# Kernel tuning notes

Measured on AMD Instinct MI355X. Metric: run time of the kernel, lower is better.

The kernel has to match this reference:

```python
import jax, jax.numpy as jnp
import numpy as np

L, E, NH, V, BS = 8, 1024, 16, 32000, 1024  # layers, embed, heads, vocab, block_size
HD = E // NH  # head dim = 64
FF = 4 * E


def layernorm(x, scale, bias, eps=1e-5):
    mu = jnp.mean(x, axis=-1, keepdims=True)
    var = jnp.var(x, axis=-1, keepdims=True)
    return (x - mu) * jax.lax.rsqrt(var + eps) * scale + bias


def setup_inputs() -> dict:
    key = jax.random.key(0)
    ks = jax.random.split(key, 16)
    s = 0.02
    B, T = 2, 1024
    return {
        "idx": jax.random.randint(ks[0], (B, T), 0, V),
        "tok_emb": jax.random.normal(ks[1], (V, E), jnp.float32) * s,
        "pos_emb": jax.random.normal(ks[2], (BS, E), jnp.float32) * s,
        "Wq": jax.random.normal(ks[3], (L, E, E), jnp.float32) * s,
        "Wk": jax.random.normal(ks[4], (L, E, E), jnp.float32) * s,
        "Wv": jax.random.normal(ks[5], (L, E, E), jnp.float32) * s,
        "Wo": jax.random.normal(ks[6], (L, E, E), jnp.float32) * s,
        "bo": jnp.zeros((L, E), jnp.float32),
        "ln1_s": jnp.ones((L, E), jnp.float32),
        "ln1_b": jnp.zeros((L, E), jnp.float32),
        "W1": jax.random.normal(ks[7], (L, E, FF), jnp.float32) * s,
        "b1": jnp.zeros((L, FF), jnp.float32),
        "W2": jax.random.normal(ks[8], (L, FF, E), jnp.float32) * s,
        "b2": jnp.zeros((L, E), jnp.float32),
        "ln2_s": jnp.ones((L, E), jnp.float32),
        "ln2_b": jnp.zeros((L, E), jnp.float32),
        "lnf_s": jnp.ones((E,), jnp.float32),
        "lnf_b": jnp.zeros((E,), jnp.float32),
        "lm_w": jax.random.normal(ks[9], (E, V), jnp.float32) * s,
        "lm_b": jnp.zeros((V,), jnp.float32),
    }


def reference(idx, tok_emb, pos_emb, Wq, Wk, Wv, Wo, bo, ln1_s, ln1_b,
              W1, b1, W2, b2, ln2_s, ln2_b, lnf_s, lnf_b, lm_w, lm_b):
    B, T = idx.shape
    x = tok_emb[idx] + pos_emb[:T]  # [B,T,E]
    causal = jnp.triu(jnp.ones((T, T), bool), 1)  # True above diagonal -> masked
    scale = 1.0 / jnp.sqrt(jnp.asarray(HD, x.dtype))
    for l in range(L):
        h = layernorm(x, ln1_s[l], ln1_b[l])
        q = (h @ Wq[l]).reshape(B, T, NH, HD)
        k = (h @ Wk[l]).reshape(B, T, NH, HD)
        v = (h @ Wv[l]).reshape(B, T, NH, HD)
        scores = jnp.einsum("bthd,bshd->bhts", q, k) * scale  # [B,H,T,T]
        scores = jnp.where(causal, -jnp.inf, scores)
        attn = jax.nn.softmax(scores, axis=-1)
        o = jnp.einsum("bhts,bshd->bthd", attn, v).reshape(B, T, E)
        x = x + o @ Wo[l] + bo[l]
        h2 = layernorm(x, ln2_s[l], ln2_b[l])
        x = x + jax.nn.gelu(h2 @ W1[l] + b1[l], approximate=False) @ W2[l] + b2[l]
    x = layernorm(x, lnf_s, lnf_b)
    logits = x @ lm_w + lm_b  # [B,T,V]
    return logits
```

## Files before the change

### kernel.cpp

```cpp
#include <hip/hip_runtime.h>

#define EDIM 1024
#define NHEADS 16
#define HDIM 64
#define TSEQ 1024
#define NBATCH 2
#define MROWS 2048
#define FFDIM 4096
#define NLAYERS 8
#define VOCAB 32000
#define QKVN 3072

typedef __attribute__((ext_vector_type(4))) float f32x4;
typedef __attribute__((ext_vector_type(8))) short short8;

__device__ __forceinline__ unsigned short f2bf(float f) {
    union { float f; unsigned u; } v; v.f = f;
    unsigned r = v.u + 0x7fffu + ((v.u >> 16) & 1u);
    return (unsigned short)(r >> 16);
}

__device__ __forceinline__ f32x4 mfma_bf16(short8 a, short8 b, f32x4 c) {
    return __builtin_amdgcn_mfma_f32_16x16x32_bf16(a, b, c, 0, 0, 0);
}

__device__ __forceinline__ void gload16(const unsigned short* g, unsigned short* l) {
    __builtin_amdgcn_global_load_lds(
        (const __attribute__((address_space(1))) unsigned int*)g,
        (__attribute__((address_space(3))) unsigned int*)l, 16, 0, 0);
}

__global__ __launch_bounds__(256) void embed_kernel(
    const int* __restrict__ idx, const float* __restrict__ tok,
    const float* __restrict__ pos, float* __restrict__ x)
{
    int row = blockIdx.x;
    int t = row & (TSEQ - 1);
    int tokid = idx[row];
    const float* tp = tok + (size_t)tokid * EDIM;
    const float* pp = pos + (size_t)t * EDIM;
    float* xp = x + (size_t)row * EDIM;
    int c = threadIdx.x * 4;
    f32x4 a = *(const f32x4*)(tp + c);
    f32x4 b = *(const f32x4*)(pp + c);
    *(f32x4*)(xp + c) = a + b;
}

__device__ __forceinline__ void ln_store(
    f32x4 v, int tid, const float* __restrict__ sc, const float* __restrict__ bi,
    unsigned short* __restrict__ hrow)
{
    float sum = v[0] + v[1] + v[2] + v[3];
    float sq = v[0]*v[0] + v[1]*v[1] + v[2]*v[2] + v[3]*v[3];
    #pragma unroll
    for (int m = 1; m <= 32; m <<= 1) { sum += __shfl_xor(sum, m); sq += __shfl_xor(sq, m); }
    __shared__ float sh[8];
    int w = tid >> 6;
    if ((tid & 63) == 0) { sh[w] = sum; sh[4 + w] = sq; }
    __syncthreads();
    sum = sh[0] + sh[1] + sh[2] + sh[3];
    sq  = sh[4] + sh[5] + sh[6] + sh[7];
    float mu = sum * (1.0f / EDIM);
    float inv = rsqrtf(sq * (1.0f / EDIM) - mu * mu + 1e-5f);
    int c = tid * 4;
    unsigned o0 = (unsigned)f2bf((v[0] - mu) * inv * sc[c + 0] + bi[c + 0])
                | ((unsigned)f2bf((v[1] - mu) * inv * sc[c + 1] + bi[c + 1]) << 16);
    unsigned o1 = (unsigned)f2bf((v[2] - mu) * inv * sc[c + 2] + bi[c + 2])
                | ((unsigned)f2bf((v[3] - mu) * inv * sc[c + 3] + bi[c + 3]) << 16);
    unsigned* hp = (unsigned*)(hrow + c);
    hp[0] = o0; hp[1] = o1;
}

__global__ __launch_bounds__(256) void ln_kernel(
    const float* __restrict__ x, const float* __restrict__ sc,
    const float* __restrict__ bi, unsigned short* __restrict__ h)
{
    int row = blockIdx.x, tid = threadIdx.x;
    f32x4 v = *(const f32x4*)(x + (size_t)row * EDIM + tid * 4);
    ln_store(v, tid, sc, bi, h + (size_t)row * EDIM);
}

template<int KZ>
__global__ __launch_bounds__(256) void reduce_ln_kernel(
    const float* __restrict__ part, const float* __restrict__ bias,
    float* __restrict__ x, const float* __restrict__ sc,
    const float* __restrict__ bi, unsigned short* __restrict__ h)
{
    int row = blockIdx.x, tid = threadIdx.x;
    int c = tid * 4;
    f32x4 s = *(const f32x4*)(x + (size_t)row * EDIM + c);
    s += *(const f32x4*)(bias + c);
    #pragma unroll
    for (int kz = 0; kz < KZ; ++kz)
        s += *(const f32x4*)(part + ((size_t)kz * MROWS + row) * EDIM + c);
    *(f32x4*)(x + (size_t)row * EDIM + c) = s;
    ln_store(s, tid, sc, bi, h + (size_t)row * EDIM);
}

__device__ __forceinline__ void conv_tile(
    const float* __restrict__ W, unsigned short* __restrict__ WT,
    int Kdim, int Ndim, int k0, int n0, int tid)
{
    __shared__ unsigned short T[64][72];
    int r = tid >> 4, c4 = (tid & 15) * 4;
    #pragma unroll
    for (int i = 0; i < 4; ++i) {
        f32x4 v = *(const f32x4*)(W + (size_t)(k0 + r + 16 * i) * Ndim + n0 + c4);
        T[c4 + 0][r + 16 * i] = f2bf(v[0]);
        T[c4 + 1][r + 16 * i] = f2bf(v[1]);
        T[c4 + 2][r + 16 * i] = f2bf(v[2]);
        T[c4 + 3][r + 16 * i] = f2bf(v[3]);
    }
    __syncthreads();
    int nr = tid >> 2, kc = (tid & 3) * 16;
    short8 o0 = *(const short8*)&T[nr][kc];
    short8 o1 = *(const short8*)&T[nr][kc + 8];
    *(short8*)(WT + (size_t)(n0 + nr) * Kdim + k0 + kc)     = o0;
    *(short8*)(WT + (size_t)(n0 + nr) * Kdim + k0 + kc + 8) = o1;
}

__global__ __launch_bounds__(256) void wconv_layer_kernel(
    const float* __restrict__ Wq, const float* __restrict__ Wk,
    const float* __restrict__ Wv, const float* __restrict__ Wo,
    const float* __restrict__ W1, const float* __restrict__ W2,
    unsigned short* __restrict__ qkvT, unsigned short* __restrict__ woT,
    unsigned short* __restrict__ w1T, unsigned short* __restrict__ w2T)
{
    int bid = blockIdx.x, tid = threadIdx.x;
    if (bid < 768) {
        int wsel = bid >> 8, t = bid & 255;
        const float* src = wsel == 0 ? Wq : (wsel == 1 ? Wk : Wv);
        conv_tile(src, qkvT + (size_t)wsel * EDIM * EDIM, EDIM, EDIM,
                  (t & 15) * 64, (t >> 4) * 64, tid);
    } else if (bid < 1024) {
        int t = bid - 768;
        conv_tile(Wo, woT, EDIM, EDIM, (t & 15) * 64, (t >> 4) * 64, tid);
    } else if (bid < 2048) {
        int t = bid - 1024;
        conv_tile(W1, w1T, EDIM, FFDIM, (t & 15) * 64, (t >> 4) * 64, tid);
    } else {
        int t = bid - 2048;
        conv_tile(W2, w2T, FFDIM, EDIM, (t >> 4) * 64, (t & 15) * 64, tid);
    }
}

__global__ __launch_bounds__(256) void wconv_kernel(
    const float* __restrict__ W, unsigned short* __restrict__ WT, int Kdim, int Ndim)
{
    conv_tile(W, WT, Kdim, Ndim, blockIdx.x * 64, blockIdx.y * 64, threadIdx.x);
}

template<int EPI>
__global__ __launch_bounds__(256, 3) void gemm128(
    const unsigned short* __restrict__ A, const unsigned short* __restrict__ WT,
    const float* __restrict__ bias, float* __restrict__ Cf,
    unsigned short* __restrict__ Cb, int Ndim, int Kdim,
    int ntiles, int nwg, int kspan)
{
    __shared__ __align__(16) unsigned short A_lds[128][64];
    __shared__ __align__(16) unsigned short B_lds[128][64];
    int tid = threadIdx.x;
    int q8 = nwg >> 3;
    int swz = (int)(blockIdx.x & 7) * q8 + (int)(blockIdx.x >> 3);
    int bm0 = (swz / ntiles) * 128, bn0 = (swz % ntiles) * 128;
    int kz = blockIdx.y;
    int lane = tid & 63, w = tid >> 6;
    int wr = w >> 1, wc = w & 1;
    int r16 = lane & 15, cc = lane >> 4;
    int lrow = lane >> 3;
    int lcol = ((lane & 7) ^ lrow) * 8;
    int sw = r16 & 7;

    f32x4 acc[4][4];
    #pragma unroll
    for (int m = 0; m < 4; ++m)
        #pragma unroll
        for (int n = 0; n < 4; ++n) acc[m][n] = {0.f, 0.f, 0.f, 0.f};

    int kbeg = kz * kspan, kend = kbeg + kspan;
    for (int k0 = kbeg; k0 < kend; k0 += 64) {
        #pragma unroll
        for (int i = 0; i < 4; ++i) {
            int c = i * 4 + w;
            gload16(A + (size_t)(bm0 + c * 8 + lrow) * Kdim + k0 + lcol,
                    (unsigned short*)A_lds + c * 512);
            gload16(WT + (size_t)(bn0 + c * 8 + lrow) * Kdim + k0 + lcol,
                    (unsigned short*)B_lds + c * 512);
        }
        __syncthreads();
        #pragma unroll
        for (int kh = 0; kh < 2; ++kh) {
            short8 af[4], bfr[4];
            #pragma unroll
            for (int m = 0; m < 4; ++m)
                af[m] = *(const short8*)&A_lds[wr * 64 + m * 16 + r16][((kh * 4 + cc) ^ sw) * 8];
            #pragma unroll
            for (int n = 0; n < 4; ++n)
                bfr[n] = *(const short8*)&B_lds[wc * 64 + n * 16 + r16][((kh * 4 + cc) ^ sw) * 8];
            #pragma unroll
            for (int m = 0; m < 4; ++m)
                #pragma unroll
                for (int n = 0; n < 4; ++n)
                    acc[m][n] = mfma_bf16(af[m], bfr[n], acc[m][n]);
        }
        __syncthreads();
    }

    #pragma unroll
    for (int m = 0; m < 4; ++m) {
        #pragma unroll
        for (int n = 0; n < 4; ++n) {
            #pragma unroll
            for (int j = 0; j < 4; ++j) {
                int row = bm0 + wr * 64 + m * 16 + cc * 4 + j;
                int col = bn0 + wc * 64 + n * 16 + r16;
                float vv = acc[m][n][j];
                if constexpr (EPI == 0)
                    Cb[(size_t)row * Ndim + col] = f2bf(vv);
                else
                    (Cf + (size_t)kz * MROWS * Ndim)[(size_t)row * Ndim + col] = vv;
            }
        }
    }
}

template<int EPI>
__global__ __launch_bounds__(512, 2) void gemm_p3(
    const unsigned short* __restrict__ A, const unsigned short* __restrict__ WT,
    const float* __restrict__ bias, float* __restrict__ Cf,
    unsigned short* __restrict__ Cb, int Ndim, int Kdim, int mtiles, int ntiles)
{
    __shared__ __align__(16) unsigned short LDS[3][24576];
    const int tid = threadIdx.x;
    const int nwg = mtiles * ntiles, q8 = nwg >> 3;
    const int swz = (int)(blockIdx.x & 7) * q8 + (int)(blockIdx.x >> 3);
    const int bn0 = (swz / mtiles) * 256, bm0 = (swz % mtiles) * 128;
    const int lane = tid & 63, w = tid >> 6;
    const int wr = w >> 2, wc = w & 3;
    const int r16 = lane & 15, cc = lane >> 4;
    const int lrow = lane >> 3;
    const int lcol = ((lane & 7) ^ lrow) * 8;
    const int sw = r16 & 7;

    f32x4 acc[4][4];
    #pragma unroll
    for (int m = 0; m < 4; ++m)
        #pragma unroll
        for (int n = 0; n < 4; ++n) acc[m][n] = {0.f, 0.f, 0.f, 0.f};

    const int nk = Kdim >> 6;

    auto STAGE = [&](int t, int bufidx) {
        int k0 = t * 64;
        unsigned short* buf = &LDS[bufidx][0];
        #pragma unroll
        for (int i = 0; i < 2; ++i) {
            int c = i * 8 + w;
            gload16(A + (size_t)(bm0 + c * 8 + lrow) * Kdim + k0 + lcol, buf + c * 512);
        }
        #pragma unroll
        for (int i = 0; i < 4; ++i) {
            int c = i * 8 + w;
            gload16(WT + (size_t)(bn0 + c * 8 + lrow) * Kdim + k0 + lcol, buf + 8192 + c * 512);
        }
    };

    STAGE(0, 0);
    STAGE(1, 1);
    asm volatile("s_waitcnt vmcnt(6)" ::: "memory");
    __builtin_amdgcn_sched_barrier(0);
    __builtin_amdgcn_s_barrier();
    __builtin_amdgcn_sched_barrier(0);

    int cur = 0;
    for (int t = 0; t < nk; ++t) {
        if (t + 2 < nk) STAGE(t + 2, cur == 0 ? 2 : cur - 1);
        const unsigned short* Abuf = &LDS[cur][0];
        const unsigned short* Bbuf = &LDS[cur][8192];
        #pragma unroll
        for (int kh = 0; kh < 2; ++kh) {
            short8 af[4], bfr[4];
            #pragma unroll
            for (int m = 0; m < 4; ++m)
                af[m] = *(const short8*)&Abuf[(wr * 64 + m * 16 + r16) * 64 + ((kh * 4 + cc) ^ sw) * 8];
            #pragma unroll
            for (int n = 0; n < 4; ++n)
                bfr[n] = *(const short8*)&Bbuf[(wc * 64 + n * 16 + r16) * 64 + ((kh * 4 + cc) ^ sw) * 8];
            __builtin_amdgcn_s_setprio(1);
            #pragma unroll
            for (int m = 0; m < 4; ++m)
                #pragma unroll
                for (int n = 0; n < 4; ++n)
                    acc[m][n] = mfma_bf16(af[m], bfr[n], acc[m][n]);
            __builtin_amdgcn_s_setprio(0);
        }
        if (t + 1 < nk) {
            if (t + 2 < nk) asm volatile("s_waitcnt vmcnt(6)" ::: "memory");
            else            asm volatile("s_waitcnt vmcnt(0)" ::: "memory");
            __builtin_amdgcn_sched_barrier(0);
            __builtin_amdgcn_s_barrier();
            __builtin_amdgcn_sched_barrier(0);
            asm volatile("" ::: "memory");
        }
        cur = cur == 2 ? 0 : cur + 1;
    }

    #pragma unroll
    for (int m = 0; m < 4; ++m) {
        #pragma unroll
        for (int n = 0; n < 4; ++n) {
            #pragma unroll
            for (int j = 0; j < 4; ++j) {
                int row = bm0 + wr * 64 + m * 16 + cc * 4 + j;
                int col = bn0 + wc * 64 + n * 16 + r16;
                float vv = acc[m][n][j] + bias[col];
                if constexpr (EPI == 2) {
                    vv = 0.5f * vv * (1.0f + erff(vv * 0.70710678118654752f));
                    Cb[(size_t)row * Ndim + col] = f2bf(vv);
                } else {
                    Cf[(size_t)row * Ndim + col] = vv;
                }
            }
        }
    }
}

__global__ __launch_bounds__(256) void attn_kernel(
    const unsigned short* __restrict__ qkv, unsigned short* __restrict__ o)
{
    __shared__ __align__(16) unsigned short K_lds[64][72];
    __shared__ __align__(16) unsigned short VT_lds[64][72];
    __shared__ __align__(16) unsigned short P_lds[4][16][72];

    int qt = blockIdx.x, head = blockIdx.y, bb = blockIdx.z;
    int tid = threadIdx.x, w = tid >> 6, lane = tid & 63;
    int r16 = lane & 15, cc = lane >> 4;
    size_t base = ((size_t)bb * TSEQ) * QKVN + head * HDIM;
    const unsigned short* q = qkv + base;
    const unsigned short* k = qkv + base + EDIM;
    const unsigned short* v = qkv + base + 2 * EDIM;
    size_t obase = ((size_t)bb * TSEQ) * EDIM + head * HDIM;
    int qbase = qt * 64;

    const unsigned short* qp = q + (size_t)(qbase + w * 16 + r16) * QKVN;
    short8 aq0 = *(const short8*)(qp + cc * 8);
    short8 aq1 = *(const short8*)(qp + 32 + cc * 8);

    f32x4 oacc[4];
    float mrow[4], lrow[4];
    #pragma unroll
    for (int n = 0; n < 4; ++n) oacc[n] = {0.f, 0.f, 0.f, 0.f};
    #pragma unroll
    for (int j = 0; j < 4; ++j) { mrow[j] = -1e30f; lrow[j] = 0.f; }

    int krow = tid >> 2, kch = tid & 3;
    int vkey2 = (tid & 31) * 2, vdh = tid >> 5;

    for (int kt = 0; kt <= qt; ++kt) {
        int kbase = kt * 64;
        const unsigned short* kp = k + (size_t)(kbase + krow) * QKVN + kch * 16;
        short8 kv0 = *(const short8*)kp;
        short8 kv1 = *(const short8*)(kp + 8);
        *(short8*)&K_lds[krow][kch * 16]     = kv0;
        *(short8*)&K_lds[krow][kch * 16 + 8] = kv1;
        const unsigned short* vp0 = v + (size_t)(kbase + vkey2) * QKVN + vdh * 8;
        short8 v0 = *(const short8*)vp0;
        short8 v1 = *(const short8*)(vp0 + QKVN);
        #pragma unroll
        for (int i = 0; i < 8; ++i) {
            unsigned pk = (unsigned)(unsigned short)v0[i]
                        | ((unsigned)(unsigned short)v1[i] << 16);
            *(unsigned*)&VT_lds[vdh * 8 + i][vkey2] = pk;
        }
        __syncthreads();

        f32x4 s[4];
        #pragma unroll
        for (int n = 0; n < 4; ++n) {
            short8 bk0 = *(const short8*)&K_lds[n * 16 + r16][cc * 8];
            short8 bk1 = *(const short8*)&K_lds[n * 16 + r16][32 + cc * 8];
            f32x4 z = {0.f, 0.f, 0.f, 0.f};
            z = mfma_bf16(aq0, bk0, z);
            z = mfma_bf16(aq1, bk1, z);
            s[n] = z;
        }
        bool diag = (kt == qt);
        float p[4][4];
        #pragma unroll
        for (int n = 0; n < 4; ++n)
            #pragma unroll
            for (int j = 0; j < 4; ++j) {
                float sv = s[n][j] * 0.125f;
                if (diag && (kbase + n * 16 + r16 > qbase + w * 16 + cc * 4 + j)) sv = -1e30f;
                p[n][j] = sv;
            }
        float alpha[4];
        #pragma unroll
        for (int j = 0; j < 4; ++j) {
            float tmax = fmaxf(fmaxf(p[0][j], p[1][j]), fmaxf(p[2][j], p[3][j]));
            #pragma unroll
            for (int mm = 1; mm <= 8; mm <<= 1) tmax = fmaxf(tmax, __shfl_xor(tmax, mm));
            float mnew = fmaxf(mrow[j], tmax);
            alpha[j] = __expf(mrow[j] - mnew);
            mrow[j] = mnew;
            float tsum = 0.f;
            #pragma unroll
            for (int n = 0; n < 4; ++n) {
                float pe = __expf(p[n][j] - mnew);
                p[n][j] = pe;
                tsum += pe;
            }
            #pragma unroll
            for (int mm = 1; mm <= 8; mm <<= 1) tsum += __shfl_xor(tsum, mm);
            lrow[j] = lrow[j] * alpha[j] + tsum;
        }
        #pragma unroll
        for (int n = 0; n < 4; ++n) {
            #pragma unroll
            for (int j = 0; j < 4; ++j) {
                P_lds[w][cc * 4 + j][n * 16 + r16] = f2bf(p[n][j]);
                oacc[n][j] *= alpha[j];
            }
        }
        short8 pa0 = *(const short8*)&P_lds[w][r16][cc * 8];
        short8 pa1 = *(const short8*)&P_lds[w][r16][32 + cc * 8];
        #pragma unroll
        for (int n = 0; n < 4; ++n) {
            short8 bv0 = *(const short8*)&VT_lds[n * 16 + r16][cc * 8];
            short8 bv1 = *(const short8*)&VT_lds[n * 16 + r16][32 + cc * 8];
            oacc[n] = mfma_bf16(pa0, bv0, oacc[n]);
            oacc[n] = mfma_bf16(pa1, bv1, oacc[n]);
        }
        __syncthreads();
    }
    float rl[4];
    #pragma unroll
    for (int j = 0; j < 4; ++j) rl[j] = 1.0f / lrow[j];
    #pragma unroll
    for (int n = 0; n < 4; ++n)
        #pragma unroll
        for (int j = 0; j < 4; ++j) {
            int row = qbase + w * 16 + cc * 4 + j;
            o[obase + (size_t)row * EDIM + n * 16 + r16] = f2bf(oacc[n][j] * rl[j]);
        }
}

extern "C" void kernel_launch(void* const* d_in, const int* in_sizes, int n_in,
                              void* d_out, int out_size, void* d_ws, size_t ws_size,
                              hipStream_t stream) {
    const int*   idx     = (const int*)d_in[0];
    const float* tok_emb = (const float*)d_in[1];
    const float* pos_emb = (const float*)d_in[2];
    const float* Wq      = (const float*)d_in[3];
    const float* Wk      = (const float*)d_in[4];
    const float* Wv      = (const float*)d_in[5];
    const float* Wo      = (const float*)d_in[6];
    const float* bo      = (const float*)d_in[7];
    const float* ln1_s   = (const float*)d_in[8];
    const float* ln1_b   = (const float*)d_in[9];
    const float* W1      = (const float*)d_in[10];
    const float* b1      = (const float*)d_in[11];
    const float* W2      = (const float*)d_in[12];
    const float* b2      = (const float*)d_in[13];
    const float* ln2_s   = (const float*)d_in[14];
    const float* ln2_b   = (const float*)d_in[15];
    const float* lnf_s   = (const float*)d_in[16];
    const float* lnf_b   = (const float*)d_in[17];
    const float* lm_w    = (const float*)d_in[18];
    const float* lm_b    = (const float*)d_in[19];
    float* out = (float*)d_out;

    char* ws = (char*)d_ws;
    float*          x    = (float*)ws;
    unsigned short* h    = (unsigned short*)(ws + (8  << 20));
    unsigned short* qkv  = (unsigned short*)(ws + (12 << 20));
    unsigned short* ao   = (unsigned short*)(ws + (24 << 20));
    unsigned short* ff   = (unsigned short*)(ws + (28 << 20));
    unsigned short* qkvT = (unsigned short*)(ws + (44 << 20));
    unsigned short* woT  = (unsigned short*)(ws + (50 << 20));
    unsigned short* w1T  = (unsigned short*)(ws + (52 << 20));
    unsigned short* w2T  = (unsigned short*)(ws + (60 << 20));
    unsigned short* lmT  = (unsigned short*)(ws + (68 << 20));
    float*          part = (float*)(ws + (68 << 20));

    dim3 blk(256);
    embed_kernel<<<MROWS, blk, 0, stream>>>(idx, tok_emb, pos_emb, x);
    ln_kernel<<<MROWS, blk, 0, stream>>>(x, ln1_s, ln1_b, h);

    for (int l = 0; l < NLAYERS; ++l) {
        size_t eo = (size_t)l * EDIM * EDIM;
        wconv_layer_kernel<<<3072, blk, 0, stream>>>(
            Wq + eo, Wk + eo, Wv + eo, Wo + eo,
            W1 + (size_t)l * EDIM * FFDIM, W2 + (size_t)l * FFDIM * EDIM,
            qkvT, woT, w1T, w2T);

        gemm128<0><<<dim3(384, 1), blk, 0, stream>>>(h, qkvT, nullptr, nullptr, qkv, QKVN, EDIM, 24, 384, EDIM);
        attn_kernel<<<dim3(TSEQ / 64, NHEADS, NBATCH), blk, 0, stream>>>(qkv, ao);
        gemm128<4><<<dim3(128, 4), blk, 0, stream>>>(ao, woT, nullptr, part, nullptr, EDIM, EDIM, 8, 128, 256);
        reduce_ln_kernel<4><<<MROWS, blk, 0, stream>>>(part, bo + l * EDIM, x, ln2_s + l * EDIM, ln2_b + l * EDIM, h);
        gemm_p3<2><<<dim3(256, 1), dim3(512), 0, stream>>>(h, w1T, b1 + l * FFDIM, nullptr, ff, FFDIM, EDIM, 16, 16);
        gemm128<4><<<dim3(128, 4), blk, 0, stream>>>(ff, w2T, nullptr, part, nullptr, EDIM, FFDIM, 8, 128, 1024);
        if (l < NLAYERS - 1)
            reduce_ln_kernel<4><<<MROWS, blk, 0, stream>>>(part, b2 + l * EDIM, x, ln1_s + (l + 1) * EDIM, ln1_b + (l + 1) * EDIM, h);
        else
            reduce_ln_kernel<4><<<MROWS, blk, 0, stream>>>(part, b2 + l * EDIM, x, lnf_s, lnf_b, h);
    }
    wconv_kernel<<<dim3(16, 500), blk, 0, stream>>>(lm_w, lmT, EDIM, VOCAB);
    gemm_p3<3><<<dim3(2000, 1), dim3(512), 0, stream>>>(h, lmT, lm_b, out, nullptr, VOCAB, EDIM, 16, 125);
}
```

Baseline: 1.550 ms.

## Widen attention key tiles with lazy rescaling and add 128x256 LM-head GEMM

The attention kernel now processes 128-key tiles instead of 64. It folds the softmax scale into an exp2 base, and it skips rescaling the output accumulator when the running max grows by less than a threshold. It also raises wave priority around the MFMA blocks. Separately, the LM-head projection switches to a new 128x256-tile GEMM with swizzled LDS and XCD-aware block remapping, in place of the previous 512-thread kernel. These changes aim to cut per-tile softmax and sync overhead and raise MFMA reuse. The cost is more registers and LDS, plus wasted masked work on the diagonal tile when the query-tile index is even.

```diff
diff --git a/kernel.cpp b/kernel.cpp
--- a/kernel.cpp
+++ b/kernel.cpp
@@ -10,6 +10,7 @@
 #define NLAYERS 8
 #define VOCAB 32000
 #define QKVN 3072
+#define SC2 0.18033688011112042f
 
 typedef __attribute__((ext_vector_type(4))) float f32x4;
 typedef __attribute__((ext_vector_type(8))) short short8;
@@ -325,12 +326,83 @@
     }
 }
 
+__global__ __launch_bounds__(256, 2) void gemm_wide_lm(
+    const unsigned short* __restrict__ A, const unsigned short* __restrict__ WT,
+    const float* __restrict__ bias, float* __restrict__ Cf,
+    int Ndim, int Kdim, int mtiles, int ntiles)
+{
+    __shared__ __align__(16) unsigned short A_lds[128][64];
+    __shared__ __align__(16) unsigned short B_lds[256][64];
+    int tid = threadIdx.x;
+    int nwg = mtiles * ntiles;
+    int q8 = nwg >> 3;
+    int swz = (int)(blockIdx.x & 7) * q8 + (int)(blockIdx.x >> 3);
+    int bn0 = (swz / mtiles) * 256, bm0 = (swz % mtiles) * 128;
+    int lane = tid & 63, w = tid >> 6;
+    int wr = w >> 1, wc = w & 1;
+    int r16 = lane & 15, cc = lane >> 4;
+    int lrow = lane >> 3;
+    int lcol = ((lane & 7) ^ lrow) * 8;
+    int sw = r16 & 7;
+
+    f32x4 acc[4][8];
+    #pragma unroll
+    for (int m = 0; m < 4; ++m)
+        #pragma unroll
+        for (int n = 0; n < 8; ++n) acc[m][n] = {0.f, 0.f, 0.f, 0.f};
+
+    for (int k0 = 0; k0 < Kdim; k0 += 64) {
+        #pragma unroll
+        for (int i = 0; i < 4; ++i) {
+            int c = i * 4 + w;
+            gload16(A + (size_t)(bm0 + c * 8 + lrow) * Kdim + k0 + lcol,
+                    (unsigned short*)A_lds + c * 512);
+        }
+        #pragma unroll
+        for (int i = 0; i < 8; ++i) {
+            int c = i * 4 + w;
+            gload16(WT + (size_t)(bn0 + c * 8 + lrow) * Kdim + k0 + lcol,
+                    (unsigned short*)B_lds + c * 512);
+        }
+        __syncthreads();
+        #pragma unroll
+        for (int kh = 0; kh < 2; ++kh) {
+            short8 af[4], bfr[8];
+            #pragma unroll
+            for (int m = 0; m < 4; ++m)
+                af[m] = *(const short8*)&A_lds[wr * 64 + m * 16 + r16][((kh * 4 + cc) ^ sw) * 8];
+            #pragma unroll
+            for (int n = 0; n < 8; ++n)
+                bfr[n] = *(const short8*)&B_lds[wc * 128 + n * 16 + r16][((kh * 4 + cc) ^ sw) * 8];
+            #pragma unroll
+            for (int m = 0; m < 4; ++m)
+                #pragma unroll
+                for (int n = 0; n < 8; ++n)
+                    acc[m][n] = mfma_bf16(af[m], bfr[n], acc[m][n]);
+        }
+        __syncthreads();
+    }
+
+    #pragma unroll
+    for (int m = 0; m < 4; ++m) {
+        #pragma unroll
+        for (int n = 0; n < 8; ++n) {
+            #pragma unroll
+            for (int j = 0; j < 4; ++j) {
+                int row = bm0 + wr * 64 + m * 16 + cc * 4 + j;
+                int col = bn0 + wc * 128 + n * 16 + r16;
+                Cf[(size_t)row * Ndim + col] = acc[m][n][j] + bias[col];
+            }
+        }
+    }
+}
+
 __global__ __launch_bounds__(256) void attn_kernel(
     const unsigned short* __restrict__ qkv, unsigned short* __restrict__ o)
 {
-    __shared__ __align__(16) unsigned short K_lds[64][72];
-    __shared__ __align__(16) unsigned short VT_lds[64][72];
-    __shared__ __align__(16) unsigned short P_lds[4][16][72];
+    __shared__ __align__(16) unsigned short K_lds[128][72];
+    __shared__ __align__(16) unsigned short VT_lds[64][136];
+    __shared__ __align__(16) unsigned short P_lds[4][16][136];
 
     int qt = blockIdx.x, head = blockIdx.y, bb = blockIdx.z;
     int tid = threadIdx.x, w = tid >> 6, lane = tid & 63;
@@ -347,36 +419,41 @@
     short8 aq1 = *(const short8*)(qp + 32 + cc * 8);
 
     f32x4 oacc[4];
-    float mrow[4], lrow[4];
+    float m2[4], lrow[4];
     #pragma unroll
     for (int n = 0; n < 4; ++n) oacc[n] = {0.f, 0.f, 0.f, 0.f};
     #pragma unroll
-    for (int j = 0; j < 4; ++j) { mrow[j] = -1e30f; lrow[j] = 0.f; }
-
-    int krow = tid >> 2, kch = tid & 3;
-    int vkey2 = (tid & 31) * 2, vdh = tid >> 5;
-
-    for (int kt = 0; kt <= qt; ++kt) {
-        int kbase = kt * 64;
-        const unsigned short* kp = k + (size_t)(kbase + krow) * QKVN + kch * 16;
-        short8 kv0 = *(const short8*)kp;
-        short8 kv1 = *(const short8*)(kp + 8);
-        *(short8*)&K_lds[krow][kch * 16]     = kv0;
-        *(short8*)&K_lds[krow][kch * 16 + 8] = kv1;
-        const unsigned short* vp0 = v + (size_t)(kbase + vkey2) * QKVN + vdh * 8;
-        short8 v0 = *(const short8*)vp0;
-        short8 v1 = *(const short8*)(vp0 + QKVN);
+    for (int j = 0; j < 4; ++j) { m2[j] = -1e30f; lrow[j] = 0.f; }
+
+    int krow = tid >> 1, kch = (tid & 1) * 32;
+    int vk2 = (tid & 63) * 2, vdb = (tid >> 6) * 16;
+
+    int nkt = (qt + 2) >> 1;
+    for (int kt = 0; kt < nkt; ++kt) {
+        int kbase = kt * 128;
+        const unsigned short* kp = k + (size_t)(kbase + krow) * QKVN + kch;
+        *(short8*)&K_lds[krow][kch]      = *(const short8*)kp;
+        *(short8*)&K_lds[krow][kch + 8]  = *(const short8*)(kp + 8);
+        *(short8*)&K_lds[krow][kch + 16] = *(const short8*)(kp + 16);
+        *(short8*)&K_lds[krow][kch + 24] = *(const short8*)(kp + 24);
+        const unsigned short* vp0 = v + (size_t)(kbase + vk2) * QKVN + vdb;
+        short8 v0a = *(const short8*)vp0;
+        short8 v0b = *(const short8*)(vp0 + 8);
+        short8 v1a = *(const short8*)(vp0 + QKVN);
+        short8 v1b = *(const short8*)(vp0 + QKVN + 8);
         #pragma unroll
         for (int i = 0; i < 8; ++i) {
-            unsigned pk = (unsigned)(unsigned short)v0[i]
-                        | ((unsigned)(unsigned short)v1[i] << 16);
-            *(unsigned*)&VT_lds[vdh * 8 + i][vkey2] = pk;
+            *(unsigned*)&VT_lds[vdb + i][vk2] =
+                (unsigned)(unsigned short)v0a[i] | ((unsigned)(unsigned short)v1a[i] << 16);
+            *(unsigned*)&VT_lds[vdb + 8 + i][vk2] =
+                (unsigned)(unsigned short)v0b[i] | ((unsigned)(unsigned short)v1b[i] << 16);
         }
         __syncthreads();
 
-        f32x4 s[4];
-        #pragma unroll
-        for (int n = 0; n < 4; ++n) {
+        f32x4 s[8];
+        __builtin_amdgcn_s_setprio(1);
+        #pragma unroll
+        for (int n = 0; n < 8; ++n) {
             short8 bk0 = *(const short8*)&K_lds[n * 16 + r16][cc * 8];
             short8 bk1 = *(const short8*)&K_lds[n * 16 + r16][32 + cc * 8];
             f32x4 z = {0.f, 0.f, 0.f, 0.f};
@@ -384,53 +461,73 @@
             z = mfma_bf16(aq1, bk1, z);
             s[n] = z;
         }
-        bool diag = (kt == qt);
-        float p[4][4];
-        #pragma unroll
-        for (int n = 0; n < 4; ++n)
+        __builtin_amdgcn_s_setprio(0);
+        int myrow = qbase + w * 16 + cc * 4;
+        #pragma unroll
+        for (int n = 0; n < 8; ++n) {
+            int key = kbase + n * 16 + r16;
             #pragma unroll
             for (int j = 0; j < 4; ++j) {
-                float sv = s[n][j] * 0.125f;
-                if (diag && (kbase + n * 16 + r16 > qbase + w * 16 + cc * 4 + j)) sv = -1e30f;
-                p[n][j] = sv;
+                float sv = s[n][j] * SC2;
+                if (key > myrow + j) sv = -1e30f;
+                s[n][j] = sv;
             }
-        float alpha[4];
+        }
+        float tmax[4];
         #pragma unroll
         for (int j = 0; j < 4; ++j) {
-            float tmax = fmaxf(fmaxf(p[0][j], p[1][j]), fmaxf(p[2][j], p[3][j]));
-            #pragma unroll
-            for (int mm = 1; mm <= 8; mm <<= 1) tmax = fmaxf(tmax, __shfl_xor(tmax, mm));
-            float mnew = fmaxf(mrow[j], tmax);
-            alpha[j] = __expf(mrow[j] - mnew);
-            mrow[j] = mnew;
-            float tsum = 0.f;
-            #pragma unroll
-            for (int n = 0; n < 4; ++n) {
-                float pe = __expf(p[n][j] - mnew);
-                p[n][j] = pe;
-                tsum += pe;
+            float t0 = fmaxf(fmaxf(s[0][j], s[1][j]), fmaxf(s[2][j], s[3][j]));
+            float t1 = fmaxf(fmaxf(s[4][j], s[5][j]), fmaxf(s[6][j], s[7][j]));
+            float tm = fmaxf(t0, t1);
+            #pragma unroll
+            for (int mm = 1; mm <= 8; mm <<= 1) tm = fmaxf(tm, __shfl_xor(tm, mm));
+            tmax[j] = tm;
+        }
+        bool defer = (tmax[0] - m2[0] <= 11.5f) && (tmax[1] - m2[1] <= 11.5f)
+                  && (tmax[2] - m2[2] <= 11.5f) && (tmax[3] - m2[3] <= 11.5f);
+        if (!__all(defer)) {
+            #pragma unroll
+            for (int j = 0; j < 4; ++j) {
+                float mnew = fmaxf(m2[j], tmax[j]);
+                float al = exp2f(m2[j] - mnew);
+                m2[j] = mnew;
+                lrow[j] *= al;
+                #pragma unroll
+                for (int n = 0; n < 4; ++n) oacc[n][j] *= al;
             }
-            #pragma unroll
-            for (int mm = 1; mm <= 8; mm <<= 1) tsum += __shfl_xor(tsum, mm);
-            lrow[j] = lrow[j] * alpha[j] + tsum;
-        }
+        }
+        #pragma unroll
+        for (int j = 0; j < 4; ++j) {
+            float ts = 0.f;
+            #pragma unroll
+            for (int n = 0; n < 8; ++n) {
+                float pe = exp2f(s[n][j] - m2[j]);
+                s[n][j] = pe;
+                ts += pe;
+            }
+            #pragma unroll
+            for (int mm = 1; mm <= 8; mm <<= 1) ts += __shfl_xor(ts, mm);
+            lrow[j] += ts;
+        }
+        #pragma unroll
+        for (int n = 0; n < 8; ++n)
+            #pragma unroll
+            for (int j = 0; j < 4; ++j)
+                P_lds[w][cc * 4 + j][n * 16 + r16] = f2bf(s[n][j]);
+        short8 pa[4];
+        #pragma unroll
+        for (int qq = 0; qq < 4; ++qq)
+            pa[qq] = *(const short8*)&P_lds[w][r16][qq * 32 + cc * 8];
+        __builtin_amdgcn_s_setprio(1);
         #pragma unroll
         for (int n = 0; n < 4; ++n) {
             #pragma unroll
-            for (int j = 0; j < 4; ++j) {
-                P_lds[w][cc * 4 + j][n * 16 + r16] = f2bf(p[n][j]);
-                oacc[n][j] *= alpha[j];
+            for (int qq = 0; qq < 4; ++qq) {
+                short8 bv = *(const short8*)&VT_lds[n * 16 + r16][qq * 32 + cc * 8];
+                oacc[n] = mfma_bf16(pa[qq], bv, oacc[n]);
             }
         }
-        short8 pa0 = *(const short8*)&P_lds[w][r16][cc * 8];
-        short8 pa1 = *(const short8*)&P_lds[w][r16][32 + cc * 8];
-        #pragma unroll
-        for (int n = 0; n < 4; ++n) {
-            short8 bv0 = *(const short8*)&VT_lds[n * 16 + r16][cc * 8];
-            short8 bv1 = *(const short8*)&VT_lds[n * 16 + r16][32 + cc * 8];
-            oacc[n] = mfma_bf16(pa0, bv0, oacc[n]);
-            oacc[n] = mfma_bf16(pa1, bv1, oacc[n]);
-        }
+        __builtin_amdgcn_s_setprio(0);
         __syncthreads();
     }
     float rl[4];
@@ -506,5 +603,5 @@
             reduce_ln_kernel<4><<<MROWS, blk, 0, stream>>>(part, b2 + l * EDIM, x, lnf_s, lnf_b, h);
     }
     wconv_kernel<<<dim3(16, 500), blk, 0, stream>>>(lm_w, lmT, EDIM, VOCAB);
-    gemm_p3<3><<<dim3(2000, 1), dim3(512), 0, stream>>>(h, lmT, lm_b, out, nullptr, VOCAB, EDIM, 16, 125);
-}
+    gemm_wide_lm<<<dim3(2000, 1), blk, 0, stream>>>(h, lmT, lm_b, out, VOCAB, EDIM, 16, 125);
+}
```

Measured after the change: 1.521 ms. About the same (-1.9%).
